# Kernel optimization log

Measured on AMD Instinct MI355X. Metric: run time of the kernel, lower is better.

## Reference

```python
import jax, jax.numpy as jnp
import numpy as np

N, B, PER, NELEM, E = 8192, 32, 256, 5, 131072
H, F, G, L = 128, 128, 50, 6
NC = B * NELEM
CUTOFF = 10.0
LOG2 = float(np.log(2.0))


def ssp(x):
    return jax.nn.softplus(x) - LOG2


def setup_inputs() -> dict:
    key = jax.random.key(0)
    ks = jax.random.split(key, 24)
    pos = jax.random.normal(ks[0], (N, 3), dtype=jnp.float32) * 2.0
    # component structure: node n in graph g gets element slot n % NELEM
    comp_id = (jnp.arange(N) // PER) * NELEM + (jnp.arange(N) % NELEM)
    comps_z = jax.random.randint(ks[1], (NC,), 1, 100)
    z = comps_z[comp_id]
    # edges restricted to within a graph (mimics radius_graph with batch)
    eg = jax.random.randint(ks[2], (E,), 0, B)
    src = eg * PER + jax.random.randint(ks[3], (E,), 0, PER)
    dst = eg * PER + jax.random.randint(ks[4], (E,), 0, PER)
    edge_index = jnp.stack([src, dst], axis=0)
    s = 0.05
    p = lambda k, shp: jax.random.normal(k, shp, dtype=jnp.float32) * s
    return {
        "pos": pos,
        "emb_table": p(ks[5], (100, H)),
        "mlp_w1": p(ks[6], (L, G, F)),
        "mlp_b1": jnp.zeros((L, F), jnp.float32),
        "mlp_w2": p(ks[7], (L, F, F)),
        "mlp_b2": jnp.zeros((L, F), jnp.float32),
        "cf_lin1_w": p(ks[8], (L, H, F)),
        "cf_lin2_w": p(ks[9], (L, F, H)),
        "cf_lin2_b": jnp.zeros((L, H), jnp.float32),
        "int_lin_w": p(ks[10], (L, H, H)),
        "int_lin_b": jnp.zeros((L, H), jnp.float32),
        "out_w1": p(ks[11], (H, H // 2)),
        "out_b1": jnp.zeros((H // 2,), jnp.float32),
        "out_w2": p(ks[12], (H // 2, 1)),
        "out_b2": jnp.zeros((1,), jnp.float32),
        "z": z,
        "comp_id": comp_id,
        "edge_index": edge_index,
        "comps_z": comps_z,
    }


def reference(pos, emb_table, mlp_w1, mlp_b1, mlp_w2, mlp_b2,
              cf_lin1_w, cf_lin2_w, cf_lin2_b, int_lin_w, int_lin_b,
              out_w1, out_b1, out_w2, out_b2,
              z, comp_id, edge_index, comps_z):
    src, dst = edge_index[0], edge_index[1]
    # edge distances and Gaussian smearing
    ew = jnp.linalg.norm(pos[src] - pos[dst], axis=-1)              # [E]
    offset = jnp.linspace(0.0, CUTOFF, G)
    coeff = -0.5 / (offset[1] - offset[0]) ** 2
    edge_attr = jnp.exp(coeff * (ew[:, None] - offset[None, :]) ** 2)  # [E,G]
    # cutoff envelope used by CFConv
    C = CUTOFF / (1e-10 + ew ** 2) - 1.0                            # [E]

    h = emb_table[z]                 # [N,H] node features (fixed across blocks)
    types = emb_table[comps_z]       # [NC,H] component features

    counts = jax.ops.segment_sum(jnp.ones((N,), jnp.float32), comp_id,
                                 num_segments=NC)                   # [NC]
    batch_c = jnp.arange(NC) // NELEM

    for i in range(L):
        # edge filter MLP * cutoff weight
        W = ssp(edge_attr @ mlp_w1[i] + mlp_b1[i]) @ mlp_w2[i] + mlp_b2[i]
        W = W * C[:, None]                                          # [E,F]
        xh = h @ cf_lin1_w[i]                                       # [N,F]
        msg = xh[src] * W                                           # [E,F]
        agg = jax.ops.segment_sum(msg, dst, num_segments=N)         # [N,F]
        # per-component mean pooling
        comp = jax.ops.segment_sum(agg, comp_id, num_segments=NC) / counts[:, None]
        x = comp @ cf_lin2_w[i] + cf_lin2_b[i]                      # [NC,H]
        x = ssp(x) @ int_lin_w[i] + int_lin_b[i]
        types = types + x

    # readout (num_tasks=1, n_seq=None branch)
    h2 = ssp(types @ out_w1 + out_b1)
    per_comp = h2 @ out_w2 + out_b2                                 # [NC,1]
    out = jax.ops.segment_sum(per_comp, batch_c, num_segments=B)    # [B,1]
    return out
```

## Files before the change

kernel.cpp:

```cpp
#include <hip/hip_runtime.h>


#define NNODES 8192
#define NGRAPH 32
#define NELEM  5
#define NEDGE  131072
#define HD     128
#define FD     128
#define GD     50
#define LL     6
#define NC     160
#define NZ     100
#define CUT    10.0f
#define LOG2_  0.69314718055994531f

#define CAP    1024
#define PADE   (NC * CAP)
#define PADG   (PADE / 64)
#define GPITCH 72
#define TPITCH 136
#define CSTR   16

#define W1F_ELEMS (LL * 2 * 8 * 64 * 8)
#define W2F_ELEMS (LL * 4 * 8 * 64 * 8)
#define NSCATB   (NEDGE / 256)
#define NFRAGB   ((W1F_ELEMS + W2F_ELEMS) / 256)
#define NXHZB    (LL * NZ / 2)

typedef _Float16 half8 __attribute__((ext_vector_type(8)));
typedef float floatx4 __attribute__((ext_vector_type(4)));

__device__ __forceinline__ float ssp(float x) {
    float m = fmaxf(x, 0.0f);
    float z = __expf(-fabsf(x));
    return m + __logf(1.0f + z) - LOG2_;
}

__global__ __launch_bounds__(256) void setup_kernel(
    const float* __restrict__ pos, const int* __restrict__ ei,
    const int* __restrict__ comp_id, const int* __restrict__ z,
    const float* __restrict__ w1, const float* __restrict__ w2,
    const float* __restrict__ emb, const float* __restrict__ cf1,
    int* __restrict__ counts, int* __restrict__ cursor,
    float* __restrict__ ew_s, float* __restrict__ c_s, int* __restrict__ zsrc_s,
    _Float16* __restrict__ w1f, _Float16* __restrict__ w2f, float* __restrict__ xh_z)
{
    int bx = blockIdx.x;
    int tid = threadIdx.x;
    if (bx < NSCATB) {
        int e = bx * 256 + tid;
        int s = ei[e], d = ei[NEDGE + e];
        float dx = pos[3*s]   - pos[3*d];
        float dy = pos[3*s+1] - pos[3*d+1];
        float dz = pos[3*s+2] - pos[3*d+2];
        float d2 = dx*dx + dy*dy + dz*dz;
        float ew = sqrtf(d2);
        float C  = CUT / (1e-10f + d2) - 1.0f;
        int cid = comp_id[d];
        int idx = cid * CAP + atomicAdd(&cursor[cid * CSTR], 1);
        ew_s[idx] = ew; c_s[idx] = C; zsrc_s[idx] = z[s];
        if (e < NNODES) atomicAdd(&counts[comp_id[e]], 1);
        return;
    }
    int fx = bx - NSCATB;
    if (fx < NFRAGB) {
        int idx = fx * 256 + tid;
        if (idx < W1F_ELEMS) {
            int j = idx & 7, lane = (idx >> 3) & 63, tcg = (idx >> 9) & 7;
            int kb = (idx >> 12) & 1, l = idx >> 13;
            int k = kb * 32 + (lane >> 4) * 8 + j;
            int col = tcg * 16 + (lane & 15);
            float v = (k < GD) ? w1[(l * GD + k) * FD + col] : 0.0f;
            w1f[idx] = (_Float16)v;
        } else {
            int id2 = idx - W1F_ELEMS;
            int j = id2 & 7, lane = (id2 >> 3) & 63, tcg = (id2 >> 9) & 7;
            int kb = (id2 >> 12) & 3, l = id2 >> 14;
            int k = kb * 32 + (lane >> 4) * 8 + j;
            int col = tcg * 16 + (lane & 15);
            w2f[id2] = (_Float16)w2[(l * FD + k) * FD + col];
        }
    } else {
        int bz = fx - NFRAGB;
        int l = bz / (NZ / 2);
        int zv = (bz % (NZ / 2)) * 2 + (tid >> 7);
        int f = tid & 127;
        const float* h = emb + zv * HD;
        const float* w = cf1 + l * HD * FD;
        float acc = 0.0f;
        #pragma unroll 8
        for (int k = 0; k < HD; ++k) acc = fmaf(h[k], w[k * FD + f], acc);
        xh_z[(l * NZ + zv) * FD + f] = acc;
    }
}

__global__ __launch_bounds__(256, 4) void edge_kernel(
    const float* __restrict__ ew_s, const float* __restrict__ c_s,
    const int* __restrict__ zsrc_s,
    const _Float16* __restrict__ w1f, const float* __restrict__ b1_,
    const _Float16* __restrict__ w2f, const float* __restrict__ b2_,
    const float* __restrict__ xh_z, float* __restrict__ comp_acc)
{
    __shared__ __align__(16) _Float16 smem[64 * TPITCH];
    __shared__ float ce_l[64];
    __shared__ int   zs_l[64];

    const int tid  = threadIdx.x;
    const int lane = tid & 63;
    const int l15  = lane & 15;
    const int quad = lane >> 4;
    const int fq   = __builtin_amdgcn_readfirstlane(tid >> 6);
    const int l    = blockIdx.y;
    const int cid  = blockIdx.x % NC;
    const int gg   = blockIdx.x / NC;
    const int g0   = cid * CAP + gg * 64;

    const float delta = CUT / (GD - 1);
    const float coeff = -0.5f / (delta * delta);

    const float ce = c_s[g0 + lane];
    if (__all(ce == 0.0f)) return;
    if (tid < 64) {
        ce_l[tid] = ce;
        zs_l[tid] = zsrc_s[g0 + tid];
    }
    const int colbase = fq * 32 + l15;
    const float b1c0 = b1_[l * FD + colbase];
    const float b1c1 = b1_[l * FD + colbase + 16];
    const float b2c0 = b2_[l * FD + colbase];
    const float b2c1 = b2_[l * FD + colbase + 16];

    {
        const float ewr = ew_s[g0 + lane];
        half8 ga, gb;
        #pragma unroll
        for (int i = 0; i < 8; ++i) {
            float d0 = ewr - (fq * 16 + i) * delta;
            float d1 = ewr - (fq * 16 + 8 + i) * delta;
            ga[i] = (_Float16)__expf(coeff * d0 * d0);
            gb[i] = (_Float16)__expf(coeff * d1 * d1);
        }
        *(half8*)&smem[lane * GPITCH + fq * 16]     = ga;
        *(half8*)&smem[lane * GPITCH + fq * 16 + 8] = gb;
    }
    __syncthreads();

    floatx4 accT[4][2];
    #pragma unroll
    for (int tr = 0; tr < 4; ++tr) {
        accT[tr][0] = (floatx4){b1c0, b1c0, b1c0, b1c0};
        accT[tr][1] = (floatx4){b1c1, b1c1, b1c1, b1c1};
    }
    const half8* w1fp = (const half8*)w1f;
    #pragma unroll
    for (int kb = 0; kb < 2; ++kb) {
        half8 bf0 = w1fp[((l * 2 + kb) * 8 + fq * 2 + 0) * 64 + lane];
        half8 bf1 = w1fp[((l * 2 + kb) * 8 + fq * 2 + 1) * 64 + lane];
        #pragma unroll
        for (int tr = 0; tr < 4; ++tr) {
            half8 af = *(const half8*)&smem[(tr * 16 + l15) * GPITCH + kb * 32 + quad * 8];
            accT[tr][0] = __builtin_amdgcn_mfma_f32_16x16x32_f16(af, bf0, accT[tr][0], 0, 0, 0);
            accT[tr][1] = __builtin_amdgcn_mfma_f32_16x16x32_f16(af, bf1, accT[tr][1], 0, 0, 0);
        }
    }
    __syncthreads();

    #pragma unroll
    for (int tr = 0; tr < 4; ++tr) {
        #pragma unroll
        for (int tcl = 0; tcl < 2; ++tcl) {
            #pragma unroll
            for (int r = 0; r < 4; ++r) {
                float v = ssp(accT[tr][tcl][r]);
                smem[(tr * 16 + quad * 4 + r) * TPITCH + fq * 32 + tcl * 16 + l15] = (_Float16)v;
            }
        }
    }
    __syncthreads();

    floatx4 accW[4][2];
    #pragma unroll
    for (int tr = 0; tr < 4; ++tr) {
        accW[tr][0] = (floatx4){b2c0, b2c0, b2c0, b2c0};
        accW[tr][1] = (floatx4){b2c1, b2c1, b2c1, b2c1};
    }
    const half8* w2fp = (const half8*)w2f;
    #pragma unroll
    for (int kb = 0; kb < 4; ++kb) {
        half8 bf0 = w2fp[((l * 4 + kb) * 8 + fq * 2 + 0) * 64 + lane];
        half8 bf1 = w2fp[((l * 4 + kb) * 8 + fq * 2 + 1) * 64 + lane];
        #pragma unroll
        for (int tr = 0; tr < 4; ++tr) {
            half8 af = *(const half8*)&smem[(tr * 16 + l15) * TPITCH + kb * 32 + quad * 8];
            accW[tr][0] = __builtin_amdgcn_mfma_f32_16x16x32_f16(af, bf0, accW[tr][0], 0, 0, 0);
            accW[tr][1] = __builtin_amdgcn_mfma_f32_16x16x32_f16(af, bf1, accW[tr][1], 0, 0, 0);
        }
    }

    float s0 = 0.0f, s1 = 0.0f;
    #pragma unroll
    for (int tr = 0; tr < 4; ++tr) {
        #pragma unroll
        for (int r = 0; r < 4; ++r) {
            const int e = tr * 16 + quad * 4 + r;
            const float cee = ce_l[e];
            const float* xr = xh_z + (l * NZ + zs_l[e]) * FD + colbase;
            s0 += accW[tr][0][r] * cee * xr[0];
            s1 += accW[tr][1][r] * cee * xr[16];
        }
    }
    s0 += __shfl_xor(s0, 16); s0 += __shfl_xor(s0, 32);
    s1 += __shfl_xor(s1, 16); s1 += __shfl_xor(s1, 32);
    float* cacc = comp_acc + (l * NC + cid) * FD + fq * 32;
    if (quad == 0) {
        atomicAdd(&cacc[l15],      s0);
        atomicAdd(&cacc[l15 + 16], s1);
    }
}

__global__ __launch_bounds__(128) void comp_kernel(
    const float* __restrict__ comp_acc, const int* __restrict__ counts,
    const float* __restrict__ cf2w, const float* __restrict__ cf2b,
    const float* __restrict__ intw, const float* __restrict__ intb,
    float* __restrict__ types_acc)
{
    int c = blockIdx.x, l = blockIdx.y, f = threadIdx.x;
    __shared__ float comp[FD];
    __shared__ float sx[FD];
    comp[f] = comp_acc[(l * NC + c) * FD + f] / (float)counts[c];
    __syncthreads();
    float acc = cf2b[l * HD + f];
    const float* w = cf2w + l * FD * HD;
    #pragma unroll 8
    for (int k = 0; k < FD; ++k) acc = fmaf(comp[k], w[k * HD + f], acc);
    sx[f] = ssp(acc);
    __syncthreads();
    float acc2 = intb[l * HD + f];
    const float* wi = intw + l * HD * HD;
    #pragma unroll 8
    for (int k = 0; k < HD; ++k) acc2 = fmaf(sx[k], wi[k * HD + f], acc2);
    atomicAdd(&types_acc[c * HD + f], acc2);
}

__global__ __launch_bounds__(64) void readout_kernel(
    const float* __restrict__ types_acc, const float* __restrict__ emb,
    const int* __restrict__ comps_z,
    const float* __restrict__ w1, const float* __restrict__ b1,
    const float* __restrict__ w2, const float* __restrict__ b2,
    float* __restrict__ out)
{
    int b = blockIdx.x, lane = threadIdx.x;
    float sum = 0.0f;
    for (int cc = 0; cc < NELEM; ++cc) {
        int c = b * NELEM + cc;
        int zc = comps_z[c];
        float acc = b1[lane];
        const float* ta = types_acc + c * HD;
        const float* eb = emb + zc * HD;
        #pragma unroll 8
        for (int k = 0; k < HD; ++k) acc = fmaf(ta[k] + eb[k], w1[k * 64 + lane], acc);
        sum += ssp(acc) * w2[lane];
    }
    #pragma unroll
    for (int s = 32; s > 0; s >>= 1) sum += __shfl_xor(sum, s);
    if (lane == 0) out[b] = sum + (float)NELEM * b2[0];
}

extern "C" void kernel_launch(void* const* d_in, const int* in_sizes, int n_in,
                              void* d_out, int out_size, void* d_ws, size_t ws_size,
                              hipStream_t stream) {
    (void)in_sizes; (void)n_in; (void)out_size; (void)ws_size;
    const float* pos     = (const float*)d_in[0];
    const float* emb     = (const float*)d_in[1];
    const float* mlp_w1  = (const float*)d_in[2];
    const float* mlp_b1  = (const float*)d_in[3];
    const float* mlp_w2  = (const float*)d_in[4];
    const float* mlp_b2  = (const float*)d_in[5];
    const float* cf1     = (const float*)d_in[6];
    const float* cf2w    = (const float*)d_in[7];
    const float* cf2b    = (const float*)d_in[8];
    const float* intw    = (const float*)d_in[9];
    const float* intb    = (const float*)d_in[10];
    const float* ow1     = (const float*)d_in[11];
    const float* ob1     = (const float*)d_in[12];
    const float* ow2     = (const float*)d_in[13];
    const float* ob2     = (const float*)d_in[14];
    const int*   z       = (const int*)d_in[15];
    const int*   comp_id = (const int*)d_in[16];
    const int*   ei      = (const int*)d_in[17];
    const int*   comps_z = (const int*)d_in[18];
    float* out = (float*)d_out;

    char* ws = (char*)d_ws;
    size_t off = 0;
    auto alloc = [&](size_t bytes) -> void* {
        void* p = ws + off;
        off += (bytes + 255) & ~(size_t)255;
        return p;
    };
    float* comp_acc  = (float*)alloc((size_t)LL * NC * FD * 4);
    int*   counts    = (int*)  alloc(NC * 4);
    float* types_acc = (float*)alloc((size_t)NC * HD * 4);
    int*   cursor    = (int*)  alloc(NC * CSTR * 4);
    float* c_s       = (float*)alloc((size_t)PADE * 4);
    int*   zsrc_s    = (int*)  alloc((size_t)PADE * 4);
    size_t zero_bytes = off;
    float* ew_s     = (float*)alloc((size_t)PADE * 4);
    float* xh_z     = (float*)alloc((size_t)LL * NZ * FD * 4);
    _Float16* w1f   = (_Float16*)alloc((size_t)W1F_ELEMS * 2);
    _Float16* w2f   = (_Float16*)alloc((size_t)W2F_ELEMS * 2);

    hipMemsetAsync(d_ws, 0, zero_bytes, stream);

    setup_kernel<<<NSCATB + NFRAGB + NXHZB, 256, 0, stream>>>(
        pos, ei, comp_id, z, mlp_w1, mlp_w2, emb, cf1,
        counts, cursor, ew_s, c_s, zsrc_s, w1f, w2f, xh_z);
    edge_kernel <<<dim3(PADG, LL), 256, 0, stream>>>(ew_s, c_s, zsrc_s,
                                                     w1f, mlp_b1, w2f, mlp_b2,
                                                     xh_z, comp_acc);
    comp_kernel <<<dim3(NC, LL), 128, 0, stream>>>(comp_acc, counts, cf2w, cf2b,
                                                   intw, intb, types_acc);
    readout_kernel<<<NGRAPH, 64, 0, stream>>>(types_acc, emb, comps_z,
                                              ow1, ob1, ow2, ob2, out);
}
```

Baseline: 238.5 us.

## Precompute Gaussian smearing in setup and fuse comp and readout kernels

Computes the fp16 Gaussian edge features once in the setup scatter pass and stores them in a global buffer that the edge kernel reads directly as MFMA A fragments. This removes the per-layer exp recomputation and an LDS stage plus barrier. It also merges the per-layer component MLP and the readout into one kernel that loops over layers per component and accumulates into the output atomically. The cost is a large extra global buffer read six times, and fewer blocks in the fused tail kernel.

```diff
diff --git a/kernel.cpp b/kernel.cpp
--- a/kernel.cpp
+++ b/kernel.cpp
@@ -17,7 +17,6 @@
 #define CAP    1024
 #define PADE   (NC * CAP)
 #define PADG   (PADE / 64)
-#define GPITCH 72
 #define TPITCH 136
 #define CSTR   16
 
@@ -42,8 +41,10 @@
     const float* __restrict__ w1, const float* __restrict__ w2,
     const float* __restrict__ emb, const float* __restrict__ cf1,
     int* __restrict__ counts, int* __restrict__ cursor,
-    float* __restrict__ ew_s, float* __restrict__ c_s, int* __restrict__ zsrc_s,
-    _Float16* __restrict__ w1f, _Float16* __restrict__ w2f, float* __restrict__ xh_z)
+    float* __restrict__ c_s, int* __restrict__ zsrc_s,
+    _Float16* __restrict__ g_glob,
+    _Float16* __restrict__ w1f, _Float16* __restrict__ w2f,
+    float* __restrict__ xh_z, float* __restrict__ out)
 {
     int bx = blockIdx.x;
     int tid = threadIdx.x;
@@ -58,12 +59,26 @@
         float C  = CUT / (1e-10f + d2) - 1.0f;
         int cid = comp_id[d];
         int idx = cid * CAP + atomicAdd(&cursor[cid * CSTR], 1);
-        ew_s[idx] = ew; c_s[idx] = C; zsrc_s[idx] = z[s];
+        c_s[idx] = C; zsrc_s[idx] = z[s];
+        const float delta = CUT / (GD - 1);
+        const float coeff = -0.5f / (delta * delta);
+        _Float16* gr = g_glob + (size_t)idx * 64;
+        #pragma unroll
+        for (int kk = 0; kk < 64; kk += 8) {
+            half8 gv;
+            #pragma unroll
+            for (int j = 0; j < 8; ++j) {
+                float dd = ew - (kk + j) * delta;
+                gv[j] = (_Float16)__expf(coeff * dd * dd);
+            }
+            *(half8*)(gr + kk) = gv;
+        }
         if (e < NNODES) atomicAdd(&counts[comp_id[e]], 1);
         return;
     }
     int fx = bx - NSCATB;
     if (fx < NFRAGB) {
+        if (fx == 0 && tid < NGRAPH) out[tid] = 0.0f;
         int idx = fx * 256 + tid;
         if (idx < W1F_ELEMS) {
             int j = idx & 7, lane = (idx >> 3) & 63, tcg = (idx >> 9) & 7;
@@ -95,8 +110,8 @@
 }
 
 __global__ __launch_bounds__(256, 4) void edge_kernel(
-    const float* __restrict__ ew_s, const float* __restrict__ c_s,
-    const int* __restrict__ zsrc_s,
+    const float* __restrict__ c_s, const int* __restrict__ zsrc_s,
+    const _Float16* __restrict__ g_glob,
     const _Float16* __restrict__ w1f, const float* __restrict__ b1_,
     const _Float16* __restrict__ w2f, const float* __restrict__ b2_,
     const float* __restrict__ xh_z, float* __restrict__ comp_acc)
@@ -115,9 +130,6 @@
     const int gg   = blockIdx.x / NC;
     const int g0   = cid * CAP + gg * 64;
 
-    const float delta = CUT / (GD - 1);
-    const float coeff = -0.5f / (delta * delta);
-
     const float ce = c_s[g0 + lane];
     if (__all(ce == 0.0f)) return;
     if (tid < 64) {
@@ -130,21 +142,6 @@
     const float b2c0 = b2_[l * FD + colbase];
     const float b2c1 = b2_[l * FD + colbase + 16];
 
-    {
-        const float ewr = ew_s[g0 + lane];
-        half8 ga, gb;
-        #pragma unroll
-        for (int i = 0; i < 8; ++i) {
-            float d0 = ewr - (fq * 16 + i) * delta;
-            float d1 = ewr - (fq * 16 + 8 + i) * delta;
-            ga[i] = (_Float16)__expf(coeff * d0 * d0);
-            gb[i] = (_Float16)__expf(coeff * d1 * d1);
-        }
-        *(half8*)&smem[lane * GPITCH + fq * 16]     = ga;
-        *(half8*)&smem[lane * GPITCH + fq * 16 + 8] = gb;
-    }
-    __syncthreads();
-
     floatx4 accT[4][2];
     #pragma unroll
     for (int tr = 0; tr < 4; ++tr) {
@@ -152,18 +149,18 @@
         accT[tr][1] = (floatx4){b1c1, b1c1, b1c1, b1c1};
     }
     const half8* w1fp = (const half8*)w1f;
+    const _Float16* gp = g_glob + (size_t)g0 * 64;
     #pragma unroll
     for (int kb = 0; kb < 2; ++kb) {
         half8 bf0 = w1fp[((l * 2 + kb) * 8 + fq * 2 + 0) * 64 + lane];
         half8 bf1 = w1fp[((l * 2 + kb) * 8 + fq * 2 + 1) * 64 + lane];
         #pragma unroll
         for (int tr = 0; tr < 4; ++tr) {
-            half8 af = *(const half8*)&smem[(tr * 16 + l15) * GPITCH + kb * 32 + quad * 8];
+            half8 af = *(const half8*)(gp + (tr * 16 + l15) * 64 + kb * 32 + quad * 8);
             accT[tr][0] = __builtin_amdgcn_mfma_f32_16x16x32_f16(af, bf0, accT[tr][0], 0, 0, 0);
             accT[tr][1] = __builtin_amdgcn_mfma_f32_16x16x32_f16(af, bf1, accT[tr][1], 0, 0, 0);
         }
     }
-    __syncthreads();
 
     #pragma unroll
     for (int tr = 0; tr < 4; ++tr) {
@@ -218,52 +215,48 @@
     }
 }
 
-__global__ __launch_bounds__(128) void comp_kernel(
+__global__ __launch_bounds__(128) void comp_readout_kernel(
     const float* __restrict__ comp_acc, const int* __restrict__ counts,
     const float* __restrict__ cf2w, const float* __restrict__ cf2b,
     const float* __restrict__ intw, const float* __restrict__ intb,
-    float* __restrict__ types_acc)
+    const float* __restrict__ emb, const int* __restrict__ comps_z,
+    const float* __restrict__ ow1, const float* __restrict__ ob1,
+    const float* __restrict__ ow2, const float* __restrict__ ob2,
+    float* __restrict__ out)
 {
-    int c = blockIdx.x, l = blockIdx.y, f = threadIdx.x;
+    int c = blockIdx.x, f = threadIdx.x;
     __shared__ float comp[FD];
     __shared__ float sx[FD];
-    comp[f] = comp_acc[(l * NC + c) * FD + f] / (float)counts[c];
+    const float inv = 1.0f / (float)counts[c];
+    float tacc = emb[comps_z[c] * HD + f];
+    #pragma unroll 1
+    for (int l = 0; l < LL; ++l) {
+        comp[f] = comp_acc[(l * NC + c) * FD + f] * inv;
+        __syncthreads();
+        float acc = cf2b[l * HD + f];
+        const float* w = cf2w + l * FD * HD;
+        #pragma unroll 8
+        for (int k = 0; k < FD; ++k) acc = fmaf(comp[k], w[k * HD + f], acc);
+        sx[f] = ssp(acc);
+        __syncthreads();
+        float acc2 = intb[l * HD + f];
+        const float* wi = intw + l * HD * HD;
+        #pragma unroll 8
+        for (int k = 0; k < HD; ++k) acc2 = fmaf(sx[k], wi[k * HD + f], acc2);
+        tacc += acc2;
+        __syncthreads();
+    }
+    comp[f] = tacc;
     __syncthreads();
-    float acc = cf2b[l * HD + f];
-    const float* w = cf2w + l * FD * HD;
-    #pragma unroll 8
-    for (int k = 0; k < FD; ++k) acc = fmaf(comp[k], w[k * HD + f], acc);
-    sx[f] = ssp(acc);
-    __syncthreads();
-    float acc2 = intb[l * HD + f];
-    const float* wi = intw + l * HD * HD;
-    #pragma unroll 8
-    for (int k = 0; k < HD; ++k) acc2 = fmaf(sx[k], wi[k * HD + f], acc2);
-    atomicAdd(&types_acc[c * HD + f], acc2);
-}
-
-__global__ __launch_bounds__(64) void readout_kernel(
-    const float* __restrict__ types_acc, const float* __restrict__ emb,
-    const int* __restrict__ comps_z,
-    const float* __restrict__ w1, const float* __restrict__ b1,
-    const float* __restrict__ w2, const float* __restrict__ b2,
-    float* __restrict__ out)
-{
-    int b = blockIdx.x, lane = threadIdx.x;
-    float sum = 0.0f;
-    for (int cc = 0; cc < NELEM; ++cc) {
-        int c = b * NELEM + cc;
-        int zc = comps_z[c];
-        float acc = b1[lane];
-        const float* ta = types_acc + c * HD;
-        const float* eb = emb + zc * HD;
+    if (f < 64) {
+        float h = ob1[f];
         #pragma unroll 8
-        for (int k = 0; k < HD; ++k) acc = fmaf(ta[k] + eb[k], w1[k * 64 + lane], acc);
-        sum += ssp(acc) * w2[lane];
-    }
-    #pragma unroll
-    for (int s = 32; s > 0; s >>= 1) sum += __shfl_xor(sum, s);
-    if (lane == 0) out[b] = sum + (float)NELEM * b2[0];
+        for (int k = 0; k < HD; ++k) h = fmaf(comp[k], ow1[k * 64 + f], h);
+        float v = ssp(h) * ow2[f];
+        #pragma unroll
+        for (int s = 32; s > 0; s >>= 1) v += __shfl_xor(v, s);
+        if (f == 0) atomicAdd(&out[c / NELEM], v + ob2[0]);
+    }
 }
 
 extern "C" void kernel_launch(void* const* d_in, const int* in_sizes, int n_in,
@@ -300,26 +293,24 @@
     };
     float* comp_acc  = (float*)alloc((size_t)LL * NC * FD * 4);
     int*   counts    = (int*)  alloc(NC * 4);
-    float* types_acc = (float*)alloc((size_t)NC * HD * 4);
     int*   cursor    = (int*)  alloc(NC * CSTR * 4);
     float* c_s       = (float*)alloc((size_t)PADE * 4);
     int*   zsrc_s    = (int*)  alloc((size_t)PADE * 4);
     size_t zero_bytes = off;
-    float* ew_s     = (float*)alloc((size_t)PADE * 4);
-    float* xh_z     = (float*)alloc((size_t)LL * NZ * FD * 4);
-    _Float16* w1f   = (_Float16*)alloc((size_t)W1F_ELEMS * 2);
-    _Float16* w2f   = (_Float16*)alloc((size_t)W2F_ELEMS * 2);
+    _Float16* g_glob = (_Float16*)alloc((size_t)PADE * 64 * 2);
+    float* xh_z      = (float*)alloc((size_t)LL * NZ * FD * 4);
+    _Float16* w1f    = (_Float16*)alloc((size_t)W1F_ELEMS * 2);
+    _Float16* w2f    = (_Float16*)alloc((size_t)W2F_ELEMS * 2);
 
     hipMemsetAsync(d_ws, 0, zero_bytes, stream);
 
     setup_kernel<<<NSCATB + NFRAGB + NXHZB, 256, 0, stream>>>(
         pos, ei, comp_id, z, mlp_w1, mlp_w2, emb, cf1,
-        counts, cursor, ew_s, c_s, zsrc_s, w1f, w2f, xh_z);
-    edge_kernel <<<dim3(PADG, LL), 256, 0, stream>>>(ew_s, c_s, zsrc_s,
+        counts, cursor, c_s, zsrc_s, g_glob, w1f, w2f, xh_z, out);
+    edge_kernel <<<dim3(PADG, LL), 256, 0, stream>>>(c_s, zsrc_s, g_glob,
                                                      w1f, mlp_b1, w2f, mlp_b2,
                                                      xh_z, comp_acc);
-    comp_kernel <<<dim3(NC, LL), 128, 0, stream>>>(comp_acc, counts, cf2w, cf2b,
-                                                   intw, intb, types_acc);
-    readout_kernel<<<NGRAPH, 64, 0, stream>>>(types_acc, emb, comps_z,
-                                              ow1, ob1, ow2, ob2, out);
-}
+    comp_readout_kernel<<<NC, 128, 0, stream>>>(comp_acc, counts, cf2w, cf2b,
+                                                intw, intb, emb, comps_z,
+                                                ow1, ob1, ow2, ob2, out);
+}
```

Measured after the change: 279.0 us. 17.0% more time.
